# Optimization experiments

Measured on AMD Instinct MI355X. Metric: run time of the kernel, lower is better.

The kernel has to match this reference:

```python
import jax, jax.numpy as jnp
import numpy as np

T = 20.0
SCALE = 0.3


def setup_inputs() -> dict:
    key = jax.random.key(0)
    ks = jax.random.split(key, 6)
    B, C = 16384, 1000
    inp = {f"outputs{i+1}": jax.random.normal(ks[i], (B, C), dtype=jnp.float32) for i in range(5)}
    inp["targets"] = jax.random.randint(ks[5], (B,), 0, C, dtype=jnp.int64)
    return inp


def reference(outputs1, outputs2, outputs3, outputs4, outputs5, targets):
    # [5, B, C] stacked softmax predictions at temperature T
    preds = jnp.stack([outputs1, outputs2, outputs3, outputs4, outputs5], axis=0)
    preds = jax.nn.softmax(preds / T, axis=-1)
    # center over class dim and L2-normalize -> Pearson correlation via dot product
    v = preds - jnp.mean(preds, axis=-1, keepdims=True)            # [M,B,C]
    v = v / jnp.sqrt(jnp.sum(v * v, axis=-1, keepdims=True))       # [M,B,C]
    corr = jnp.einsum("mbc,nbc->mnb", v, v)                        # [M,M,B]
    M = preds.shape[0]
    iu, ju = jnp.triu_indices(M, k=1)
    d = jnp.sum(corr[iu, ju, :], axis=0)                            # [B] sum over pairs
    return jnp.mean(SCALE * d)
```

## Files before the change

### kernel.cpp

```cpp
#include <hip/hip_runtime.h>


#define CDIM   1000
#define C4DIM  250
#define NM     5
#define NP     15
#define T_INV  (1.0f / 20.0f)
#define SCALEF 0.3f

__global__ __launch_bounds__(256) void diversity_rows(
    const float* __restrict__ o1, const float* __restrict__ o2,
    const float* __restrict__ o3, const float* __restrict__ o4,
    const float* __restrict__ o5, float* __restrict__ ws, int B)
{
    const int lane = threadIdx.x & 63;
    const int wid  = threadIdx.x >> 6;
    const int b    = blockIdx.x * 4 + wid;
    if (b >= B) return;

    const bool act3 = lane < (C4DIM - 192);
    const size_t roff = (size_t)b * CDIM;
    const float4* base[NM] = {
        reinterpret_cast<const float4*>(o1 + roff),
        reinterpret_cast<const float4*>(o2 + roff),
        reinterpret_cast<const float4*>(o3 + roff),
        reinterpret_cast<const float4*>(o4 + roff),
        reinterpret_cast<const float4*>(o5 + roff)};

    float A[NM];
    float Bv[NP];
    #pragma unroll
    for (int i = 0; i < NM; ++i) A[i] = 0.0f;
    #pragma unroll
    for (int p = 0; p < NP; ++p) Bv[p] = 0.0f;

    float4 xb[2][NM];

    #pragma unroll
    for (int m = 0; m < NM; ++m)
        xb[0][m] = base[m][lane];

    #pragma unroll
    for (int k = 0; k < 4; ++k) {
        const int cur = k & 1;
        const int nxt = cur ^ 1;

        if (k + 1 < 4) {
            if (k + 1 == 3) {
                #pragma unroll
                for (int m = 0; m < NM; ++m) {
                    float4 t = make_float4(0.0f, 0.0f, 0.0f, 0.0f);
                    if (act3) t = base[m][lane + 192];
                    xb[nxt][m] = t;
                }
            } else {
                #pragma unroll
                for (int m = 0; m < NM; ++m)
                    xb[nxt][m] = base[m][lane + 64 * (k + 1)];
            }
        }
        __builtin_amdgcn_sched_barrier(0);

        float u[NM][4];
        #pragma unroll
        for (int m = 0; m < NM; ++m) {
            float4 v = xb[cur][m];
            u[m][0] = __expf(v.x * T_INV) - 1.0f;
            u[m][1] = __expf(v.y * T_INV) - 1.0f;
            u[m][2] = __expf(v.z * T_INV) - 1.0f;
            u[m][3] = __expf(v.w * T_INV) - 1.0f;
        }
        #pragma unroll
        for (int c = 0; c < 4; ++c) {
            #pragma unroll
            for (int i = 0; i < NM; ++i) A[i] += u[i][c];
            int p = 0;
            #pragma unroll
            for (int i = 0; i < NM; ++i) {
                #pragma unroll
                for (int j = i; j < NM; ++j) {
                    Bv[p] = fmaf(u[i][c], u[j][c], Bv[p]);
                    ++p;
                }
            }
        }
    }

    #pragma unroll
    for (int off = 32; off >= 1; off >>= 1) {
        #pragma unroll
        for (int i = 0; i < NM; ++i) A[i] += __shfl_xor(A[i], off);
        #pragma unroll
        for (int p = 0; p < NP; ++p) Bv[p] += __shfl_xor(Bv[p], off);
    }

    {
        const double Cd = (double)CDIM;
        double Ad[NM], den[NM];
        #pragma unroll
        for (int i = 0; i < NM; ++i) Ad[i] = (double)A[i];
        const int diag[NM] = {0, 5, 9, 12, 14};
        #pragma unroll
        for (int i = 0; i < NM; ++i)
            den[i] = sqrt(Cd * (double)Bv[diag[i]] - Ad[i] * Ad[i]);

        double d = 0.0;
        int p = 0;
        #pragma unroll
        for (int i = 0; i < NM; ++i) {
            #pragma unroll
            for (int j = i; j < NM; ++j) {
                if (j > i)
                    d += (Cd * (double)Bv[p] - Ad[i] * Ad[j]) / (den[i] * den[j]);
                ++p;
            }
        }
        if (lane == 0)
            ws[b] = (float)((double)SCALEF * d);
    }
}

__global__ __launch_bounds__(1024) void final_reduce(
    const float* __restrict__ ws, float* __restrict__ out, int B)
{
    __shared__ double sm[1024];
    double acc = 0.0;
    for (int i = threadIdx.x; i < B; i += 1024)
        acc += (double)ws[i];
    sm[threadIdx.x] = acc;
    __syncthreads();
    #pragma unroll
    for (int s = 512; s > 0; s >>= 1) {
        if (threadIdx.x < s) sm[threadIdx.x] += sm[threadIdx.x + s];
        __syncthreads();
    }
    if (threadIdx.x == 0)
        out[0] = (float)(sm[0] / (double)B);
}

extern "C" void kernel_launch(void* const* d_in, const int* in_sizes, int n_in,
                              void* d_out, int out_size, void* d_ws, size_t ws_size,
                              hipStream_t stream)
{
    const float* o1 = (const float*)d_in[0];
    const float* o2 = (const float*)d_in[1];
    const float* o3 = (const float*)d_in[2];
    const float* o4 = (const float*)d_in[3];
    const float* o5 = (const float*)d_in[4];

    float* ws  = (float*)d_ws;
    float* out = (float*)d_out;

    const int B = in_sizes[0] / CDIM;

    diversity_rows<<<(B + 3) / 4, 256, 0, stream>>>(o1, o2, o3, o4, o5, ws, B);
    final_reduce<<<1, 1024, 0, stream>>>(ws, out, B);
}
```

Before: 72.02 us.

## Issue all row loads upfront with inline asm and staged vmcnt waits

Replaces the double-buffered load loop with all 20 dwordx4 global loads issued at kernel start through inline asm, then consumes them in four slots gated by decreasing s_waitcnt vmcnt values. This raises memory-level parallelism per wave so more bytes are in flight. The tail slot clamps its index and masks the values instead of branching around the load. The per-row epilogue also moves from double precision to float with rsqrt, trading a little accuracy for fewer slow FP64 ops.

```diff
diff --git a/kernel.cpp b/kernel.cpp
--- a/kernel.cpp
+++ b/kernel.cpp
@@ -1,5 +1,7 @@
 #include <hip/hip_runtime.h>
 
+
+typedef float f32x4 __attribute__((ext_vector_type(4)));
 
 #define CDIM   1000
 #define C4DIM  250
@@ -7,6 +9,43 @@
 #define NP     15
 #define T_INV  (1.0f / 20.0f)
 #define SCALEF 0.3f
+
+#define GLOAD(dst, p) \
+    asm volatile("global_load_dwordx4 %0, %1, off" : "=v"(dst) : "v"(p) : "memory")
+
+#define WAITVM(N)                                              \
+    asm volatile("s_waitcnt vmcnt(" #N ")" ::: "memory");      \
+    __builtin_amdgcn_sched_barrier(0)
+
+template <bool MASKED>
+__device__ __forceinline__ void slot_accum(const f32x4* xs, bool act,
+                                           float* A, float* Bv)
+{
+    float u[NM][4];
+    #pragma unroll
+    for (int m = 0; m < NM; ++m) {
+        #pragma unroll
+        for (int c = 0; c < 4; ++c) {
+            float xv = xs[m][c];
+            if (MASKED) xv = act ? xv : 0.0f;
+            u[m][c] = __expf(xv * T_INV) - 1.0f;
+        }
+    }
+    #pragma unroll
+    for (int c = 0; c < 4; ++c) {
+        #pragma unroll
+        for (int i = 0; i < NM; ++i) A[i] += u[i][c];
+        int p = 0;
+        #pragma unroll
+        for (int i = 0; i < NM; ++i) {
+            #pragma unroll
+            for (int j = i; j < NM; ++j) {
+                Bv[p] = fmaf(u[i][c], u[j][c], Bv[p]);
+                ++p;
+            }
+        }
+    }
+}
 
 __global__ __launch_bounds__(256) void diversity_rows(
     const float* __restrict__ o1, const float* __restrict__ o2,
@@ -18,73 +57,32 @@
     const int b    = blockIdx.x * 4 + wid;
     if (b >= B) return;
 
-    const bool act3 = lane < (C4DIM - 192);
+    const bool act3 = (lane + 192) < C4DIM;
+    const int  i3   = act3 ? (lane + 192) : (C4DIM - 1);
+
     const size_t roff = (size_t)b * CDIM;
-    const float4* base[NM] = {
-        reinterpret_cast<const float4*>(o1 + roff),
-        reinterpret_cast<const float4*>(o2 + roff),
-        reinterpret_cast<const float4*>(o3 + roff),
-        reinterpret_cast<const float4*>(o4 + roff),
-        reinterpret_cast<const float4*>(o5 + roff)};
+    const float* rp[NM] = {o1 + roff, o2 + roff, o3 + roff, o4 + roff, o5 + roff};
 
-    float A[NM];
-    float Bv[NP];
+    f32x4 x0[NM], x1[NM], x2[NM], x3[NM];
+    #pragma unroll
+    for (int m = 0; m < NM; ++m) GLOAD(x0[m], rp[m] + (size_t)lane * 4);
+    #pragma unroll
+    for (int m = 0; m < NM; ++m) GLOAD(x1[m], rp[m] + (size_t)(lane + 64) * 4);
+    #pragma unroll
+    for (int m = 0; m < NM; ++m) GLOAD(x2[m], rp[m] + (size_t)(lane + 128) * 4);
+    #pragma unroll
+    for (int m = 0; m < NM; ++m) GLOAD(x3[m], rp[m] + (size_t)i3 * 4);
+
+    float A[NM], Bv[NP];
     #pragma unroll
     for (int i = 0; i < NM; ++i) A[i] = 0.0f;
     #pragma unroll
     for (int p = 0; p < NP; ++p) Bv[p] = 0.0f;
 
-    float4 xb[2][NM];
-
-    #pragma unroll
-    for (int m = 0; m < NM; ++m)
-        xb[0][m] = base[m][lane];
-
-    #pragma unroll
-    for (int k = 0; k < 4; ++k) {
-        const int cur = k & 1;
-        const int nxt = cur ^ 1;
-
-        if (k + 1 < 4) {
-            if (k + 1 == 3) {
-                #pragma unroll
-                for (int m = 0; m < NM; ++m) {
-                    float4 t = make_float4(0.0f, 0.0f, 0.0f, 0.0f);
-                    if (act3) t = base[m][lane + 192];
-                    xb[nxt][m] = t;
-                }
-            } else {
-                #pragma unroll
-                for (int m = 0; m < NM; ++m)
-                    xb[nxt][m] = base[m][lane + 64 * (k + 1)];
-            }
-        }
-        __builtin_amdgcn_sched_barrier(0);
-
-        float u[NM][4];
-        #pragma unroll
-        for (int m = 0; m < NM; ++m) {
-            float4 v = xb[cur][m];
-            u[m][0] = __expf(v.x * T_INV) - 1.0f;
-            u[m][1] = __expf(v.y * T_INV) - 1.0f;
-            u[m][2] = __expf(v.z * T_INV) - 1.0f;
-            u[m][3] = __expf(v.w * T_INV) - 1.0f;
-        }
-        #pragma unroll
-        for (int c = 0; c < 4; ++c) {
-            #pragma unroll
-            for (int i = 0; i < NM; ++i) A[i] += u[i][c];
-            int p = 0;
-            #pragma unroll
-            for (int i = 0; i < NM; ++i) {
-                #pragma unroll
-                for (int j = i; j < NM; ++j) {
-                    Bv[p] = fmaf(u[i][c], u[j][c], Bv[p]);
-                    ++p;
-                }
-            }
-        }
-    }
+    WAITVM(15);  slot_accum<false>(x0, true, A, Bv);
+    WAITVM(10);  slot_accum<false>(x1, true, A, Bv);
+    WAITVM(5);   slot_accum<false>(x2, true, A, Bv);
+    WAITVM(0);   slot_accum<true >(x3, act3, A, Bv);
 
     #pragma unroll
     for (int off = 32; off >= 1; off >>= 1) {
@@ -95,28 +93,26 @@
     }
 
     {
-        const double Cd = (double)CDIM;
-        double Ad[NM], den[NM];
-        #pragma unroll
-        for (int i = 0; i < NM; ++i) Ad[i] = (double)A[i];
+        const float Cf = (float)CDIM;
         const int diag[NM] = {0, 5, 9, 12, 14};
+        float rden[NM];
         #pragma unroll
         for (int i = 0; i < NM; ++i)
-            den[i] = sqrt(Cd * (double)Bv[diag[i]] - Ad[i] * Ad[i]);
+            rden[i] = rsqrtf(fmaf(Cf, Bv[diag[i]], -A[i] * A[i]));
 
-        double d = 0.0;
+        float d = 0.0f;
         int p = 0;
         #pragma unroll
         for (int i = 0; i < NM; ++i) {
             #pragma unroll
             for (int j = i; j < NM; ++j) {
                 if (j > i)
-                    d += (Cd * (double)Bv[p] - Ad[i] * Ad[j]) / (den[i] * den[j]);
+                    d += fmaf(Cf, Bv[p], -A[i] * A[j]) * rden[i] * rden[j];
                 ++p;
             }
         }
         if (lane == 0)
-            ws[b] = (float)((double)SCALEF * d);
+            ws[b] = SCALEF * d;
     }
 }
 
```

Result: faster. 64.29 us (-10.7%).
